# Kernel tuning notes

Hardware: AMD Instinct MI355X
Metric: run time of the kernel (lower is better)

Reference implementation:

```python
import jax, jax.numpy as jnp
import numpy as np

HEADS, KV_HEADS, HEAD_DIM = 16, 4, 128
WINDOW, ROPE_THETA, EPS = 512, 10000.0, 1e-6


def _rms_norm(x, w):
    # Gemma RMSNorm: float32 compute, scale = 1 + w
    xf = x.astype(jnp.float32)
    y = xf * jax.lax.rsqrt(jnp.mean(xf * xf, axis=-1, keepdims=True) + EPS)
    return (y * (1.0 + w.astype(jnp.float32))).astype(x.dtype)


def _rope_cos_sin(T, dtype):
    inv_freq = 1.0 / ROPE_THETA ** (jnp.arange(0, HEAD_DIM, 2, dtype=jnp.float32) / HEAD_DIM)
    pos = jnp.arange(T, dtype=jnp.float32)
    freqs = pos[:, None] * inv_freq[None, :]          # [T, Dh/2]
    emb = jnp.concatenate([freqs, freqs], axis=-1)    # [T, Dh]
    return emb.astype(dtype), emb  # cos/sin applied below


def _rotate_half(x):
    x1, x2 = jnp.split(x, 2, axis=-1)
    return jnp.concatenate([-x2, x1], axis=-1)


def setup_inputs() -> dict:
    key = jax.random.key(0)
    ks = jax.random.split(key, 7)
    B, T, D = 2, 2048, 2048
    s = lambda k, shape, fan: jax.random.normal(k, shape, jnp.float32) * (fan ** -0.5)
    return {
        "x": jax.random.normal(ks[0], (B, T, D), jnp.float32),
        "Wq": s(ks[1], (HEADS * HEAD_DIM, D), D),
        "Wk": s(ks[2], (KV_HEADS * HEAD_DIM, D), D),
        "Wv": s(ks[3], (KV_HEADS * HEAD_DIM, D), D),
        "Wo": s(ks[4], (D, HEADS * HEAD_DIM), HEADS * HEAD_DIM),
        "qn_w": jax.random.normal(ks[5], (HEAD_DIM,), jnp.float32) * 0.02,
        "kn_w": jax.random.normal(ks[6], (HEAD_DIM,), jnp.float32) * 0.02,
    }


def reference(x, Wq, Wk, Wv, Wo, qn_w, kn_w):
    B, T, D = x.shape
    H, Hkv, Dh = HEADS, KV_HEADS, HEAD_DIM
    G = H // Hkv

    q = (x @ Wq.T).reshape(B, T, H, Dh).transpose(0, 2, 1, 3)     # [B,H,T,Dh]
    k = (x @ Wk.T).reshape(B, T, Hkv, Dh).transpose(0, 2, 1, 3)   # [B,Hkv,T,Dh]
    v = (x @ Wv.T).reshape(B, T, Hkv, Dh).transpose(0, 2, 1, 3)

    q = _rms_norm(q, qn_w)
    k = _rms_norm(k, kn_w)

    emb_c, emb_f = _rope_cos_sin(T, x.dtype)
    cos = jnp.cos(emb_f).astype(x.dtype)[None, None]  # [1,1,T,Dh]
    sin = jnp.sin(emb_f).astype(x.dtype)[None, None]
    q = q * cos + _rotate_half(q) * sin
    k = k * cos + _rotate_half(k) * sin

    q = q * (Dh ** -0.5)
    qg = q.reshape(B, Hkv, G, T, Dh)

    scores = jnp.einsum('bhgtd,bhkd->bhgtk', qg.astype(jnp.float32), k.astype(jnp.float32))

    dist = jnp.arange(T)[:, None] - jnp.arange(T)[None, :]        # [T,T]
    mask = (dist >= 0) & (dist <= WINDOW)
    scores = jnp.where(mask[None, None, None], scores, jnp.finfo(jnp.float32).min)
    att = jax.nn.softmax(scores, axis=-1).astype(x.dtype)

    ctx = jnp.einsum('bhgtk,bhkd->bhgtd', att, v)                 # [B,Hkv,G,T,Dh]
    out = ctx.reshape(B, H, T, Dh).transpose(0, 2, 1, 3).reshape(B, T, H * Dh)
    return out @ Wo.T
```

## Files before the change

kernel.cpp:

```cpp
#include <hip/hip_runtime.h>
#include <stdint.h>


typedef __attribute__((ext_vector_type(8))) short bf16x8;
typedef __attribute__((ext_vector_type(4))) float f32x4;

typedef __attribute__((address_space(3))) unsigned int lds_u32;
typedef const __attribute__((address_space(1))) unsigned int glb_u32;

#define LOG2E 1.44269504088896340736f

__device__ __forceinline__ unsigned short f2bf(float f) {
  unsigned int x = __builtin_bit_cast(unsigned int, f);
  x += 0x7FFFu + ((x >> 16) & 1u);
  return (unsigned short)(x >> 16);
}

__global__ __launch_bounds__(256) void castall(const float* __restrict__ x,
                                               const float* __restrict__ wq,
                                               const float* __restrict__ wk,
                                               const float* __restrict__ wv,
                                               const float* __restrict__ wo,
                                               unsigned short* __restrict__ xb,
                                               unsigned short* __restrict__ wqkvb,
                                               unsigned short* __restrict__ wob) {
  int i = blockIdx.x * 256 + threadIdx.x;
  const float* src;
  unsigned short* dst;
  int off;
  if (i < 2097152)       { src = x;  dst = xb;              off = i; }
  else if (i < 3145728)  { src = wq; dst = wqkvb;           off = i - 2097152; }
  else if (i < 3407872)  { src = wk; dst = wqkvb + 4194304; off = i - 3145728; }
  else if (i < 3670016)  { src = wv; dst = wqkvb + 5242880; off = i - 3407872; }
  else                   { src = wo; dst = wob;             off = i - 3670016; }
  float4 v = ((const float4*)src)[off];
  uint2 o;
  o.x = (unsigned)f2bf(v.x) | ((unsigned)f2bf(v.y) << 16);
  o.y = (unsigned)f2bf(v.z) | ((unsigned)f2bf(v.w) << 16);
  ((uint2*)dst)[off] = o;
}

__global__ __launch_bounds__(256) void rope_tab(float* __restrict__ c,
                                                float* __restrict__ s) {
  int idx = blockIdx.x * 256 + threadIdx.x;
  int t = idx >> 6, i = idx & 63;
  float invf = exp2f(-(float)i * (13.287712379549449f / 64.0f));
  float a = (float)t * invf;
  c[idx] = cosf(a);
  s[idx] = sinf(a);
}

__global__ __launch_bounds__(256) void gemm_bt(const unsigned short* __restrict__ A,
                                               const unsigned short* __restrict__ B,
                                               float* __restrict__ C,
                                               int N, int K) {
  __shared__ uint8_t As[128 * 128];
  __shared__ uint8_t Bs[128 * 128];
  const int tid = threadIdx.x;
  const int lane = tid & 63;
  const int w = tid >> 6, wr = w >> 1, wc = w & 1;
  const int m0 = blockIdx.y * 128, n0 = blockIdx.x * 128;

  const int srow = lane >> 3;
  const int schunk = (lane & 7) ^ srow;

  f32x4 acc[4][4];
#pragma unroll
  for (int i = 0; i < 4; ++i)
#pragma unroll
    for (int j = 0; j < 4; ++j) acc[i][j] = f32x4{0.f, 0.f, 0.f, 0.f};

  for (int kk = 0; kk < K; kk += 64) {
    __syncthreads();
#pragma unroll
    for (int i = 0; i < 4; ++i) {
      int r0 = w * 32 + i * 8;
      const unsigned short* ag =
          A + (size_t)(m0 + r0 + srow) * K + kk + schunk * 8;
      __builtin_amdgcn_global_load_lds((glb_u32*)ag,
                                       (lds_u32*)(As + r0 * 128), 16, 0, 0);
      const unsigned short* bg =
          B + (size_t)(n0 + r0 + srow) * K + kk + schunk * 8;
      __builtin_amdgcn_global_load_lds((glb_u32*)bg,
                                       (lds_u32*)(Bs + r0 * 128), 16, 0, 0);
    }
    __syncthreads();
#pragma unroll
    for (int ks = 0; ks < 2; ++ks) {
      bf16x8 af[4], bfr[4];
#pragma unroll
      for (int mf = 0; mf < 4; ++mf) {
        int row = wr * 64 + mf * 16 + (lane & 15);
        int bo = ks * 64 + (lane >> 4) * 16;
        af[mf] = *(const bf16x8*)(As + row * 128 + (bo ^ ((row & 7) << 4)));
      }
#pragma unroll
      for (int nf = 0; nf < 4; ++nf) {
        int row = wc * 64 + nf * 16 + (lane & 15);
        int bo = ks * 64 + (lane >> 4) * 16;
        bfr[nf] = *(const bf16x8*)(Bs + row * 128 + (bo ^ ((row & 7) << 4)));
      }
#pragma unroll
      for (int mf = 0; mf < 4; ++mf)
#pragma unroll
        for (int nf = 0; nf < 4; ++nf)
          acc[mf][nf] = __builtin_amdgcn_mfma_f32_16x16x32_bf16(
              af[mf], bfr[nf], acc[mf][nf], 0, 0, 0);
    }
  }
#pragma unroll
  for (int mf = 0; mf < 4; ++mf)
#pragma unroll
    for (int nf = 0; nf < 4; ++nf) {
      int row = m0 + wr * 64 + mf * 16 + (lane >> 4) * 4;
      int col = n0 + wc * 64 + nf * 16 + (lane & 15);
#pragma unroll
      for (int r = 0; r < 4; ++r)
        C[(size_t)(row + r) * N + col] = acc[mf][nf][r];
    }
}

__global__ __launch_bounds__(256) void eplg(const float* __restrict__ qkv,
                                            const float* __restrict__ qw,
                                            const float* __restrict__ kw,
                                            const float* __restrict__ rc,
                                            const float* __restrict__ rs,
                                            unsigned short* __restrict__ qb,
                                            unsigned short* __restrict__ kb) {
  const int row = blockIdx.x;
  const int t = row & 2047;
  const int lane = threadIdx.x & 63, w = threadIdx.x >> 6;
  const float* base = qkv + (size_t)row * 3072;
  const int d0 = 2 * lane;
  const float c0 = rc[t * 64 + (d0 & 63)];
  const float c1 = rc[t * 64 + ((d0 + 1) & 63)];
  const float s0 = rs[t * 64 + (d0 & 63)];
  const float s1 = rs[t * 64 + ((d0 + 1) & 63)];
  const float sgn = (lane < 32) ? -1.0f : 1.0f;

#pragma unroll
  for (int hh = 0; hh < 4; ++hh) {
    int h = w * 4 + hh;
    float2 x = *(const float2*)(base + h * 128 + d0);
    float ss = x.x * x.x + x.y * x.y;
#pragma unroll
    for (int m = 1; m < 64; m <<= 1) ss += __shfl_xor(ss, m);
    float r = rsqrtf(ss * (1.0f / 128.0f) + 1e-6f);
    float y0 = x.x * r * (1.0f + qw[d0]);
    float y1 = x.y * r * (1.0f + qw[d0 + 1]);
    float p0 = __shfl_xor(y0, 32);
    float p1 = __shfl_xor(y1, 32);
    float o0 = (y0 * c0 + sgn * p0 * s0) * 0.08838834764831845f;
    float o1 = (y1 * c1 + sgn * p1 * s1) * 0.08838834764831845f;
    unsigned int pk = (unsigned)f2bf(o0) | ((unsigned)f2bf(o1) << 16);
    *(unsigned int*)(qb + (size_t)row * 2048 + h * 128 + d0) = pk;
  }
  {
    float2 x = *(const float2*)(base + 2048 + w * 128 + d0);
    float ss = x.x * x.x + x.y * x.y;
#pragma unroll
    for (int m = 1; m < 64; m <<= 1) ss += __shfl_xor(ss, m);
    float r = rsqrtf(ss * (1.0f / 128.0f) + 1e-6f);
    float y0 = x.x * r * (1.0f + kw[d0]);
    float y1 = x.y * r * (1.0f + kw[d0 + 1]);
    float p0 = __shfl_xor(y0, 32);
    float p1 = __shfl_xor(y1, 32);
    float o0 = y0 * c0 + sgn * p0 * s0;
    float o1 = y1 * c1 + sgn * p1 * s1;
    unsigned int pk = (unsigned)f2bf(o0) | ((unsigned)f2bf(o1) << 16);
    *(unsigned int*)(kb + (size_t)row * 512 + w * 128 + d0) = pk;
  }
}

__global__ __launch_bounds__(256) void vtrans(const float* __restrict__ qkvf,
                                              unsigned short* __restrict__ vbt) {
  __shared__ float tile[64][65];
  const int t0 = blockIdx.x * 64;
  const int d0 = blockIdx.y * 64;
  const int b = blockIdx.z;
  const int tid = threadIdx.x;
#pragma unroll
  for (int i = 0; i < 4; ++i) {
    int idx = tid + 256 * i;
    int r = idx >> 4, c4 = idx & 15;
    float4 v = *(const float4*)(qkvf + (size_t)(b * 2048 + t0 + r) * 3072 +
                                2560 + d0 + c4 * 4);
    tile[r][c4 * 4 + 0] = v.x;
    tile[r][c4 * 4 + 1] = v.y;
    tile[r][c4 * 4 + 2] = v.z;
    tile[r][c4 * 4 + 3] = v.w;
  }
  __syncthreads();
  const int dr = tid >> 2, ts = (tid & 3) * 16;
  unsigned short tmp[16];
#pragma unroll
  for (int j = 0; j < 16; ++j) tmp[j] = f2bf(tile[ts + j][dr]);
  uint4* dst = (uint4*)(vbt + (size_t)(b * 512 + d0 + dr) * 2048 + t0 + ts);
  dst[0] = *(uint4*)(tmp);
  dst[1] = *(uint4*)(tmp + 8);
}

__global__ __launch_bounds__(256) void attn(const unsigned short* __restrict__ qb,
                                            const unsigned short* __restrict__ kb,
                                            const unsigned short* __restrict__ vbt,
                                            unsigned short* __restrict__ ctxb) {
  __shared__ uint8_t Ks[64 * 256];
  __shared__ uint8_t Vs[128 * 128];
  __shared__ uint8_t Ps[4][16 * 128];
  const int qi = blockIdx.x, h = blockIdx.y, b = blockIdx.z;
  const int kvh = h >> 2;
  const int t0 = qi * 64;
  const int tid = threadIdx.x, lane = tid & 63, w = tid >> 6;

  bf16x8 qf[4];
  {
    int qrow = t0 + w * 16 + (lane & 15);
    const unsigned short* qp =
        qb + (size_t)(b * 2048 + qrow) * 2048 + h * 128 + (lane >> 4) * 8;
#pragma unroll
    for (int kc = 0; kc < 4; ++kc) qf[kc] = *(const bf16x8*)(qp + kc * 32);
  }
  f32x4 of[8];
#pragma unroll
  for (int i = 0; i < 8; ++i) of[i] = f32x4{0.f, 0.f, 0.f, 0.f};
  float m_run[4], l_run[4];
#pragma unroll
  for (int r = 0; r < 4; ++r) { m_run[r] = -1e30f; l_run[r] = 0.0f; }

  int kt0 = t0 - 512; if (kt0 < 0) kt0 = 0;
  const int nt = (t0 + 64 - kt0) >> 6;
  uint8_t* Pw = Ps[w];

  for (int it = 0; it < nt; ++it) {
    const int kt = kt0 + (it << 6);
    __syncthreads();
#pragma unroll
    for (int i = 0; i < 4; ++i) {
      int c = tid + 256 * i;
      int krow = c >> 4, kcin = c & 15;
      uint4 kv = *(const uint4*)(kb + (size_t)(b * 2048 + kt + krow) * 512 +
                                 kvh * 128 + kcin * 8);
      *(uint4*)(Ks + krow * 256 + ((kcin * 16) ^ ((krow & 7) << 4))) = kv;
      int vrow = c >> 3, vcin = c & 7;
      uint4 vv = *(const uint4*)(vbt + (size_t)(b * 512 + kvh * 128 + vrow) * 2048 +
                                 kt + vcin * 8);
      *(uint4*)(Vs + vrow * 128 + ((vcin * 16) ^ ((vrow & 7) << 4))) = vv;
    }
    __syncthreads();

    f32x4 sf[4];
#pragma unroll
    for (int nc = 0; nc < 4; ++nc) {
      f32x4 s = f32x4{0.f, 0.f, 0.f, 0.f};
      int key = nc * 16 + (lane & 15);
#pragma unroll
      for (int kc = 0; kc < 4; ++kc) {
        bf16x8 kf = *(const bf16x8*)(
            Ks + key * 256 + (((lane >> 4) * 16 + kc * 64) ^ ((key & 7) << 4)));
        s = __builtin_amdgcn_mfma_f32_16x16x32_bf16(qf[kc], kf, s, 0, 0, 0);
      }
      sf[nc] = s;
    }
#pragma unroll
    for (int nc = 0; nc < 4; ++nc) {
      int j = kt + nc * 16 + (lane & 15);
#pragma unroll
      for (int r = 0; r < 4; ++r) {
        int tq = t0 + w * 16 + (lane >> 4) * 4 + r;
        if (!((j <= tq) && (tq - j <= 512))) sf[nc][r] = -1e30f;
      }
    }
    float alpha[4];
#pragma unroll
    for (int r = 0; r < 4; ++r) {
      float mx = fmaxf(fmaxf(sf[0][r], sf[1][r]), fmaxf(sf[2][r], sf[3][r]));
      mx = fmaxf(mx, __shfl_xor(mx, 1));
      mx = fmaxf(mx, __shfl_xor(mx, 2));
      mx = fmaxf(mx, __shfl_xor(mx, 4));
      mx = fmaxf(mx, __shfl_xor(mx, 8));
      float mn = fmaxf(m_run[r], mx);
      alpha[r] = exp2f((m_run[r] - mn) * LOG2E);
      m_run[r] = mn;
    }
    float l_add[4] = {0.f, 0.f, 0.f, 0.f};
#pragma unroll
    for (int nc = 0; nc < 4; ++nc)
#pragma unroll
      for (int r = 0; r < 4; ++r) {
        float p = exp2f((sf[nc][r] - m_run[r]) * LOG2E);
        sf[nc][r] = p;
        l_add[r] += p;
      }
#pragma unroll
    for (int r = 0; r < 4; ++r) {
      float la = l_add[r];
      la += __shfl_xor(la, 1);
      la += __shfl_xor(la, 2);
      la += __shfl_xor(la, 4);
      la += __shfl_xor(la, 8);
      l_run[r] = l_run[r] * alpha[r] + la;
    }
#pragma unroll
    for (int i = 0; i < 8; ++i)
#pragma unroll
      for (int r = 0; r < 4; ++r) of[i][r] *= alpha[r];

#pragma unroll
    for (int nc = 0; nc < 4; ++nc) {
      int key = nc * 16 + (lane & 15);
#pragma unroll
      for (int r = 0; r < 4; ++r) {
        int prow = (lane >> 4) * 4 + r;
        *(unsigned short*)(Pw + prow * 128 + ((key * 2) ^ ((prow & 7) << 4))) =
            f2bf(sf[nc][r]);
      }
    }
#pragma unroll
    for (int ks = 0; ks < 2; ++ks) {
      int prow = lane & 15;
      bf16x8 pf = *(const bf16x8*)(
          Pw + prow * 128 + ((ks * 64 + (lane >> 4) * 16) ^ ((prow & 7) << 4)));
#pragma unroll
      for (int nc8 = 0; nc8 < 8; ++nc8) {
        int vrow = nc8 * 16 + (lane & 15);
        bf16x8 vf = *(const bf16x8*)(
            Vs + vrow * 128 + ((ks * 64 + (lane >> 4) * 16) ^ ((vrow & 7) << 4)));
        of[nc8] = __builtin_amdgcn_mfma_f32_16x16x32_bf16(pf, vf, of[nc8], 0, 0, 0);
      }
    }
  }
#pragma unroll
  for (int nc8 = 0; nc8 < 8; ++nc8)
#pragma unroll
    for (int r = 0; r < 4; ++r) {
      int tq = t0 + w * 16 + (lane >> 4) * 4 + r;
      int col = h * 128 + nc8 * 16 + (lane & 15);
      ctxb[(size_t)(b * 2048 + tq) * 2048 + col] = f2bf(of[nc8][r] / l_run[r]);
    }
}

extern "C" void kernel_launch(void* const* d_in, const int* in_sizes, int n_in,
                              void* d_out, int out_size, void* d_ws, size_t ws_size,
                              hipStream_t stream) {
  const float* x  = (const float*)d_in[0];
  const float* Wq = (const float*)d_in[1];
  const float* Wk = (const float*)d_in[2];
  const float* Wv = (const float*)d_in[3];
  const float* Wo = (const float*)d_in[4];
  const float* qw = (const float*)d_in[5];
  const float* kw = (const float*)d_in[6];

  uint8_t* ws = (uint8_t*)d_ws;
  if (ws_size < 131072000ull) return;
  unsigned short* xb    = (unsigned short*)(ws);
  unsigned short* wqkvb = (unsigned short*)(ws + 16777216);
  unsigned short* wob   = (unsigned short*)(ws + 29360128);
  float*          qkvf  = (float*)(ws + 37748736);
  unsigned short* qb2   = (unsigned short*)(ws + 88080384);
  unsigned short* kb2   = (unsigned short*)(ws + 104857600);
  unsigned short* vbt   = (unsigned short*)(ws + 109051904);
  unsigned short* ctxb  = (unsigned short*)(ws + 113246208);
  float*          ropec = (float*)(ws + 130023424);
  float*          ropes = (float*)(ws + 130547712);

  castall<<<18432, 256, 0, stream>>>(x, Wq, Wk, Wv, Wo, xb, wqkvb, wob);
  rope_tab<<<512, 256, 0, stream>>>(ropec, ropes);
  {
    dim3 g(3072 / 128, 4096 / 128);
    gemm_bt<<<g, 256, 0, stream>>>(xb, wqkvb, qkvf, 3072, 2048);
  }
  eplg<<<4096, 256, 0, stream>>>(qkvf, qw, kw, ropec, ropes, qb2, kb2);
  {
    dim3 g(32, 8, 2);
    vtrans<<<g, 256, 0, stream>>>(qkvf, vbt);
  }
  {
    dim3 g(32, 16, 2);
    attn<<<g, 256, 0, stream>>>(qb2, kb2, vbt, ctxb);
  }
  {
    dim3 g(2048 / 128, 4096 / 128);
    gemm_bt<<<g, 256, 0, stream>>>(ctxb, wob, (float*)d_out, 2048, 2048);
  }
}
```

Before: 327.0 us.

## Replace GEMM with double-buffered 256-row tile kernel using 8 waves

The projection GEMMs now use a templated kernel with 256xBN tiles, 512 threads and two LDS buffers, so global loads for the next K-tile run while MFMAs consume the current one. It uses explicit waitcnt/barrier scheduling and raises wave priority around the MFMA block. Larger tiles improve data reuse per byte loaded but use far more LDS and registers, and they produce fewer blocks: 192 for QKV and 256 for the output projection. That may underfill the GPU's compute units.

```diff
diff --git a/kernel.cpp b/kernel.cpp
--- a/kernel.cpp
+++ b/kernel.cpp
@@ -50,73 +50,105 @@
   s[idx] = sinf(a);
 }
 
-__global__ __launch_bounds__(256) void gemm_bt(const unsigned short* __restrict__ A,
-                                               const unsigned short* __restrict__ B,
-                                               float* __restrict__ C,
-                                               int N, int K) {
-  __shared__ uint8_t As[128 * 128];
-  __shared__ uint8_t Bs[128 * 128];
-  const int tid = threadIdx.x;
-  const int lane = tid & 63;
-  const int w = tid >> 6, wr = w >> 1, wc = w & 1;
-  const int m0 = blockIdx.y * 128, n0 = blockIdx.x * 128;
-
+template <int BN>
+__global__ __launch_bounds__(512, 2) void gemm256(const unsigned short* __restrict__ A,
+                                                  const unsigned short* __restrict__ Bm,
+                                                  float* __restrict__ C,
+                                                  int N, int K) {
+  constexpr int BSL = BN * 128;
+  __shared__ uint8_t lds[65536 + 2 * BSL];
+  const int tid = threadIdx.x, lane = tid & 63, w = tid >> 6;
+  const int wm = w >> 2, wn = w & 3;
+  const size_t m0 = (size_t)blockIdx.y * 256, n0 = (size_t)blockIdx.x * BN;
   const int srow = lane >> 3;
   const int schunk = (lane & 7) ^ srow;
 
-  f32x4 acc[4][4];
-#pragma unroll
-  for (int i = 0; i < 4; ++i)
-#pragma unroll
-    for (int j = 0; j < 4; ++j) acc[i][j] = f32x4{0.f, 0.f, 0.f, 0.f};
-
-  for (int kk = 0; kk < K; kk += 64) {
-    __syncthreads();
-#pragma unroll
-    for (int i = 0; i < 4; ++i) {
-      int r0 = w * 32 + i * 8;
-      const unsigned short* ag =
-          A + (size_t)(m0 + r0 + srow) * K + kk + schunk * 8;
-      __builtin_amdgcn_global_load_lds((glb_u32*)ag,
-                                       (lds_u32*)(As + r0 * 128), 16, 0, 0);
-      const unsigned short* bg =
-          B + (size_t)(n0 + r0 + srow) * K + kk + schunk * 8;
-      __builtin_amdgcn_global_load_lds((glb_u32*)bg,
-                                       (lds_u32*)(Bs + r0 * 128), 16, 0, 0);
-    }
-    __syncthreads();
-#pragma unroll
-    for (int ks = 0; ks < 2; ++ks) {
-      bf16x8 af[4], bfr[4];
-#pragma unroll
-      for (int mf = 0; mf < 4; ++mf) {
-        int row = wr * 64 + mf * 16 + (lane & 15);
-        int bo = ks * 64 + (lane >> 4) * 16;
-        af[mf] = *(const bf16x8*)(As + row * 128 + (bo ^ ((row & 7) << 4)));
-      }
-#pragma unroll
-      for (int nf = 0; nf < 4; ++nf) {
-        int row = wc * 64 + nf * 16 + (lane & 15);
-        int bo = ks * 64 + (lane >> 4) * 16;
-        bfr[nf] = *(const bf16x8*)(Bs + row * 128 + (bo ^ ((row & 7) << 4)));
-      }
-#pragma unroll
-      for (int mf = 0; mf < 4; ++mf)
-#pragma unroll
-        for (int nf = 0; nf < 4; ++nf)
-          acc[mf][nf] = __builtin_amdgcn_mfma_f32_16x16x32_bf16(
-              af[mf], bfr[nf], acc[mf][nf], 0, 0, 0);
-    }
-  }
-#pragma unroll
-  for (int mf = 0; mf < 4; ++mf)
-#pragma unroll
-    for (int nf = 0; nf < 4; ++nf) {
-      int row = m0 + wr * 64 + mf * 16 + (lane >> 4) * 4;
-      int col = n0 + wc * 64 + nf * 16 + (lane & 15);
+  f32x4 acc[8][BN / 64];
+#pragma unroll
+  for (int i = 0; i < 8; ++i)
+#pragma unroll
+    for (int j = 0; j < BN / 64; ++j) acc[i][j] = f32x4{0.f, 0.f, 0.f, 0.f};
+
+  const int NT = K >> 6;
+
+  auto stageA = [&](int t, int par) {
+    uint8_t* slot = lds + (par << 15);
+#pragma unroll
+    for (int j = 0; j < 4; ++j) {
+      int r0 = (j * 8 + w) * 8;
+      const unsigned short* src =
+          A + (m0 + r0 + srow) * (size_t)K + t * 64 + schunk * 8;
+      __builtin_amdgcn_global_load_lds((glb_u32*)src,
+                                       (lds_u32*)(slot + r0 * 128), 16, 0, 0);
+    }
+  };
+  auto stageB = [&](int t, int par) {
+    uint8_t* slot = lds + 65536 + par * BSL;
+#pragma unroll
+    for (int j = 0; j < BN / 64; ++j) {
+      int r0 = (j * 8 + w) * 8;
+      const unsigned short* src =
+          Bm + (n0 + r0 + srow) * (size_t)K + t * 64 + schunk * 8;
+      __builtin_amdgcn_global_load_lds((glb_u32*)src,
+                                       (lds_u32*)(slot + r0 * 128), 16, 0, 0);
+    }
+  };
+  auto compute = [&](int par, int h) {
+    const uint8_t* Asl = lds + (par << 15);
+    const uint8_t* Bsl = lds + 65536 + par * BSL;
+    bf16x8 af[8], bf[BN / 64];
+    const int x7 = lane & 7;
+    const int cx = h * 4 + (lane >> 4);
+    const int rab = wm * 128 + (lane & 15);
+    const int rbb = wn * (BN / 4) + (lane & 15);
+#pragma unroll
+    for (int mt = 0; mt < 8; ++mt)
+      af[mt] = *(const bf16x8*)(Asl + (rab + mt * 16) * 128 + ((cx ^ x7) << 4));
+#pragma unroll
+    for (int nt = 0; nt < BN / 64; ++nt)
+      bf[nt] = *(const bf16x8*)(Bsl + (rbb + nt * 16) * 128 + ((cx ^ x7) << 4));
+    __builtin_amdgcn_s_setprio(1);
+#pragma unroll
+    for (int mt = 0; mt < 8; ++mt)
+#pragma unroll
+      for (int nt = 0; nt < BN / 64; ++nt)
+        acc[mt][nt] = __builtin_amdgcn_mfma_f32_16x16x32_bf16(
+            af[mt], bf[nt], acc[mt][nt], 0, 0, 0);
+    __builtin_amdgcn_s_setprio(0);
+  };
+
+  stageA(0, 0);
+  stageB(0, 0);
+  for (int t = 0; t < NT - 1; ++t) {
+    const int p = t & 1, q = p ^ 1;
+    stageA(t + 1, q);
+    asm volatile("s_waitcnt vmcnt(4)" ::: "memory");
+    __builtin_amdgcn_s_barrier();
+    __builtin_amdgcn_sched_barrier(0);
+    compute(p, 0);
+    stageB(t + 1, q);
+    compute(p, 1);
+    asm volatile("" ::: "memory");
+    __builtin_amdgcn_s_barrier();
+    __builtin_amdgcn_sched_barrier(0);
+  }
+  {
+    const int p = (NT - 1) & 1;
+    asm volatile("s_waitcnt vmcnt(0)" ::: "memory");
+    __builtin_amdgcn_s_barrier();
+    __builtin_amdgcn_sched_barrier(0);
+    compute(p, 0);
+    compute(p, 1);
+  }
+#pragma unroll
+  for (int mt = 0; mt < 8; ++mt)
+#pragma unroll
+    for (int nt = 0; nt < BN / 64; ++nt) {
+      size_t row = m0 + wm * 128 + mt * 16 + (lane >> 4) * 4;
+      size_t col = n0 + wn * (BN / 4) + nt * 16 + (lane & 15);
 #pragma unroll
       for (int r = 0; r < 4; ++r)
-        C[(size_t)(row + r) * N + col] = acc[mf][nf][r];
+        C[(row + r) * N + col] = acc[mt][nt][r];
     }
 }
 
@@ -366,8 +398,8 @@
   castall<<<18432, 256, 0, stream>>>(x, Wq, Wk, Wv, Wo, xb, wqkvb, wob);
   rope_tab<<<512, 256, 0, stream>>>(ropec, ropes);
   {
-    dim3 g(3072 / 128, 4096 / 128);
-    gemm_bt<<<g, 256, 0, stream>>>(xb, wqkvb, qkvf, 3072, 2048);
+    dim3 g(3072 / 256, 4096 / 256);
+    gemm256<256><<<g, 512, 0, stream>>>(xb, wqkvb, qkvf, 3072, 2048);
   }
   eplg<<<4096, 256, 0, stream>>>(qkvf, qw, kw, ropec, ropes, qb2, kb2);
   {
@@ -379,7 +411,7 @@
     attn<<<g, 256, 0, stream>>>(qb2, kb2, vbt, ctxb);
   }
   {
-    dim3 g(2048 / 128, 4096 / 128);
-    gemm_bt<<<g, 256, 0, stream>>>(ctxb, wob, (float*)d_out, 2048, 2048);
-  }
-}
+    dim3 g(2048 / 128, 4096 / 256);
+    gemm256<128><<<g, 512, 0, stream>>>(ctxb, wob, (float*)d_out, 2048, 2048);
+  }
+}
```

Result: faster. 294.5 us (-9.9%).
